# Performance work log

Measured on AMD Instinct MI355X. Metric: run time of the kernel, lower is better.

## Reference

```python
import jax, jax.numpy as jnp
import numpy as np

N_NODES = 50000
N_EDGES = 800000
IN_CH = 256
HID = 32
HEADS1 = 4
OUT_CH = 64
NEG_SLOPE = 0.2


def setup_inputs() -> dict:
    key = jax.random.key(0)
    ks = jax.random.split(key, 10)
    x = jax.random.normal(ks[0], (N_NODES, IN_CH), dtype=jnp.float32)
    edge_index = jax.random.randint(ks[1], (2, N_EDGES), 0, N_NODES, dtype=jnp.int64)
    g1 = float(np.sqrt(2.0 / (IN_CH + HEADS1 * HID)))
    g2 = float(np.sqrt(2.0 / (HEADS1 * HID + OUT_CH)))
    return {
        "x": x,
        "edge_index": edge_index,
        "W1": jax.random.normal(ks[2], (IN_CH, HEADS1 * HID), dtype=jnp.float32) * g1,
        "a_src1": jax.random.normal(ks[3], (HEADS1, HID), dtype=jnp.float32) * 0.1,
        "a_dst1": jax.random.normal(ks[4], (HEADS1, HID), dtype=jnp.float32) * 0.1,
        "b1": jnp.zeros((HEADS1 * HID,), dtype=jnp.float32),
        "W2": jax.random.normal(ks[5], (HEADS1 * HID, OUT_CH), dtype=jnp.float32) * g2,
        "a_src2": jax.random.normal(ks[6], (1, OUT_CH), dtype=jnp.float32) * 0.1,
        "a_dst2": jax.random.normal(ks[7], (1, OUT_CH), dtype=jnp.float32) * 0.1,
        "b2": jnp.zeros((OUT_CH,), dtype=jnp.float32),
    }


def gat_conv(x, src, dst, W, a_s, a_d, b, concat):
    # PyG-style GATConv: per-head linear, additive attention, edge softmax over dst,
    # scatter-add aggregation.
    N = x.shape[0]
    H, C = a_s.shape
    h = (x @ W).reshape(N, H, C)                    # [N, H, C]
    as_n = jnp.einsum("nhc,hc->nh", h, a_s)         # [N, H]
    ad_n = jnp.einsum("nhc,hc->nh", h, a_d)         # [N, H]
    e = jax.nn.leaky_relu(as_n[src] + ad_n[dst], NEG_SLOPE)  # [E, H]
    # segment softmax over incoming edges of each dst node
    m = jax.lax.stop_gradient(jax.ops.segment_max(e, dst, num_segments=N))
    ex = jnp.exp(e - m[dst])
    denom = jax.ops.segment_sum(ex, dst, num_segments=N)
    alpha = ex / (denom[dst] + 1e-16)               # [E, H]
    msg = h[src] * alpha[:, :, None]                # [E, H, C]
    out = jax.ops.segment_sum(msg, dst, num_segments=N)  # [N, H, C]
    out = out.reshape(N, H * C) if concat else out.mean(axis=1)
    return out + b


def reference(x, edge_index, W1, a_src1, a_dst1, b1, W2, a_src2, a_dst2, b2):
    # eval mode: dropout(p=0.5) is identity
    src, dst = edge_index[0], edge_index[1]
    h = gat_conv(x, src, dst, W1, a_src1, a_dst1, b1, concat=True)
    h = jax.nn.relu(h)
    return gat_conv(h, src, dst, W2, a_src2, a_dst2, b2, concat=False)
```

## Files before the change

### kernel.cpp

```cpp
#include <hip/hip_runtime.h>
#include <hip/hip_fp16.h>

#define N_NODES 50000
#define N_EDGES 800000
#define IN_CH   256
#define HID     32
#define HEADS1  4
#define C1      128
#define OUT_CH  64
#define NEG     0.2f
#define INVLN2  1.4426950408889634f
#define BSHIFT  10
#define NBKT    49
#define BCAP    17664
#define N1E     144
#define N2E     80

typedef _Float16 h8 __attribute__((ext_vector_type(8)));
typedef float f32x4 __attribute__((ext_vector_type(4)));

__global__ void k_prep(const float* __restrict__ W1, const float* __restrict__ W2,
                       const float* __restrict__ a_s1, const float* __restrict__ a_d1,
                       const float* __restrict__ a_s2, const float* __restrict__ a_d2,
                       _Float16* __restrict__ Wt1e, _Float16* __restrict__ Wt2e,
                       int* __restrict__ bcur) {
    int t = blockIdx.x * 256 + threadIdx.x;
    if (blockIdx.x == 0 && threadIdx.x < NBKT) bcur[threadIdx.x] = threadIdx.x * BCAP;
    if (t < 32768) {
        int c = t >> 8, k = t & 255;
        Wt1e[(size_t)c * 256 + k] = (_Float16)W1[(size_t)k * C1 + c];
    } else if (t < 34816) {
        int i = t - 32768;
        int k = i & 255, h = (i >> 8) & 3, which = i >> 10;
        const float* av = which ? a_d1 : a_s1;
        float s = 0.f;
        for (int c = 0; c < 32; ++c)
            s = fmaf(W1[(size_t)k * C1 + h * 32 + c], av[h * 32 + c], s);
        Wt1e[(size_t)(128 + which * 4 + h) * 256 + k] = (_Float16)(s * INVLN2);
    } else if (t < 36864) {
        int i = t - 34816;
        int k = i & 255, c = 136 + (i >> 8);
        Wt1e[(size_t)c * 256 + k] = (_Float16)0.f;
    } else if (t < 45056) {
        int i = t - 36864;
        int c = i >> 7, k = i & 127;
        Wt2e[(size_t)c * 128 + k] = (_Float16)W2[(size_t)k * OUT_CH + c];
    } else if (t < 45312) {
        int i = t - 45056;
        int k = i & 127, which = i >> 7;
        const float* av = which ? a_d2 : a_s2;
        float s = 0.f;
        for (int c = 0; c < 64; ++c)
            s = fmaf(W2[(size_t)k * OUT_CH + c], av[c], s);
        Wt2e[(size_t)(64 + which) * 128 + k] = (_Float16)(s * INVLN2);
    } else if (t < 47104) {
        int i = t - 45312;
        int k = i & 127, c = 66 + (i >> 7);
        Wt2e[(size_t)c * 128 + k] = (_Float16)0.f;
    }
}

__global__ __launch_bounds__(512) void gemm1_mfma(const float* __restrict__ X,
                                                  const _Float16* __restrict__ Wt1e,
                                                  __half* __restrict__ H,
                                                  float* __restrict__ as_n,
                                                  float* __restrict__ ad_n) {
    __shared__ _Float16 As[128 * 40];
    __shared__ _Float16 Bt[N1E * 40];
    const int tid = threadIdx.x;
    const int w = tid >> 6, lane = tid & 63;
    const int row0 = blockIdx.x * 128;
    const int lr = lane & 15, lk = (lane >> 4) * 8;
    const int ar = tid >> 2, aks = (tid & 3) * 8;
    const int gr_a = row0 + ar;
    const bool arow_ok = gr_a < N_NODES;
    const int bc = tid >> 1, bq = tid & 1;
    const bool bcol_ok = tid < 2 * N1E;

    f32x4 acc[9];
#pragma unroll
    for (int n = 0; n < 9; ++n) acc[n] = (f32x4){0.f, 0.f, 0.f, 0.f};

    float4 av0 = make_float4(0.f, 0.f, 0.f, 0.f), av1 = av0;
    h8 bv0 = {}, bv1 = {};
    if (arow_ok) {
        av0 = *(const float4*)(X + (size_t)gr_a * IN_CH + aks);
        av1 = *(const float4*)(X + (size_t)gr_a * IN_CH + aks + 4);
    }
    if (bcol_ok) {
        const h8* wp = (const h8*)(Wt1e + (size_t)bc * IN_CH + bq * 16);
        bv0 = wp[0];
        bv1 = wp[1];
    }

    for (int kk = 0; kk < IN_CH; kk += 32) {
        {
            h8 hv;
            hv[0] = (_Float16)av0.x; hv[1] = (_Float16)av0.y;
            hv[2] = (_Float16)av0.z; hv[3] = (_Float16)av0.w;
            hv[4] = (_Float16)av1.x; hv[5] = (_Float16)av1.y;
            hv[6] = (_Float16)av1.z; hv[7] = (_Float16)av1.w;
            *(h8*)(&As[ar * 40 + aks]) = hv;
            if (bcol_ok) {
                *(h8*)(&Bt[bc * 40 + bq * 16]) = bv0;
                *(h8*)(&Bt[bc * 40 + bq * 16 + 8]) = bv1;
            }
        }
        __syncthreads();
        int kn = kk + 32;
        if (kn < IN_CH) {
            if (arow_ok) {
                av0 = *(const float4*)(X + (size_t)gr_a * IN_CH + kn + aks);
                av1 = *(const float4*)(X + (size_t)gr_a * IN_CH + kn + aks + 4);
            }
            if (bcol_ok) {
                const h8* wp = (const h8*)(Wt1e + (size_t)bc * IN_CH + kn + bq * 16);
                bv0 = wp[0];
                bv1 = wp[1];
            }
        }
        h8 a = *(const h8*)(&As[(w * 16 + lr) * 40 + lk]);
#pragma unroll
        for (int n = 0; n < 9; ++n) {
            h8 b = *(const h8*)(&Bt[(n * 16 + lr) * 40 + lk]);
            acc[n] = __builtin_amdgcn_mfma_f32_16x16x32_f16(a, b, acc[n], 0, 0, 0);
        }
        __syncthreads();
    }
#pragma unroll
    for (int n = 0; n < 8; ++n)
#pragma unroll
        for (int j = 0; j < 4; ++j) {
            int gr = row0 + w * 16 + (lane >> 4) * 4 + j;
            if (gr < N_NODES) H[(size_t)gr * C1 + n * 16 + lr] = __float2half(acc[n][j]);
        }
#pragma unroll
    for (int j = 0; j < 4; ++j) {
        int gr = row0 + w * 16 + (lane >> 4) * 4 + j;
        if (gr < N_NODES) {
            if (lr < 4) as_n[gr * 4 + lr] = acc[8][j];
            else if (lr < 8) ad_n[gr * 4 + (lr - 4)] = acc[8][j];
        }
    }
}

__global__ __launch_bounds__(512) void gemm2_mfma(const __half* __restrict__ A,
                                                  const _Float16* __restrict__ Wt2e,
                                                  __half* __restrict__ H,
                                                  float* __restrict__ as_n,
                                                  float* __restrict__ ad_n) {
    __shared__ _Float16 Bt[N2E * 136];
    const int tid = threadIdx.x;
    const int w = tid >> 6, lane = tid & 63;
    const int row0 = blockIdx.x * 128;
    const int lr = lane & 15, lk = (lane >> 4) * 8;
    if (tid < 160) {
        int c = tid >> 1, q = tid & 1;
        const h8* wp = (const h8*)(Wt2e + (size_t)c * C1 + q * 64);
#pragma unroll
        for (int j = 0; j < 8; ++j)
            *(h8*)(&Bt[c * 136 + q * 64 + j * 8]) = wp[j];
    }
    __syncthreads();
    f32x4 acc[5];
#pragma unroll
    for (int n = 0; n < 5; ++n) acc[n] = (f32x4){0.f, 0.f, 0.f, 0.f};
    int grow = row0 + w * 16 + lr;
    grow = grow < N_NODES ? grow : N_NODES - 1;
    const _Float16* Ah = (const _Float16*)A;
#pragma unroll
    for (int kk = 0; kk < C1; kk += 32) {
        h8 a = *(const h8*)(Ah + (size_t)grow * C1 + kk + lk);
#pragma unroll
        for (int n = 0; n < 5; ++n) {
            h8 b = *(const h8*)(&Bt[(n * 16 + lr) * 136 + kk + lk]);
            acc[n] = __builtin_amdgcn_mfma_f32_16x16x32_f16(a, b, acc[n], 0, 0, 0);
        }
    }
#pragma unroll
    for (int n = 0; n < 4; ++n)
#pragma unroll
        for (int j = 0; j < 4; ++j) {
            int gr = row0 + w * 16 + (lane >> 4) * 4 + j;
            if (gr < N_NODES) H[(size_t)gr * OUT_CH + n * 16 + lr] = __float2half(acc[n][j]);
        }
#pragma unroll
    for (int j = 0; j < 4; ++j) {
        int gr = row0 + w * 16 + (lane >> 4) * 4 + j;
        if (gr < N_NODES) {
            if (lr == 0) as_n[gr] = acc[4][j];
            else if (lr == 1) ad_n[gr] = acc[4][j];
        }
    }
}

__global__ __launch_bounds__(256) void k_bucket(const int* __restrict__ src,
                                                const int* __restrict__ dst,
                                                int* __restrict__ bcur,
                                                int* __restrict__ pairs) {
    __shared__ int cnt[4 * NBKT];
    __shared__ int base[4 * NBKT];
    const int t = threadIdx.x;
    const int w = t >> 6;
    for (int i = t; i < 4 * NBKT; i += 256) cnt[i] = 0;
    __syncthreads();
    const int e0 = blockIdx.x * 2048 + t * 8;
    int s[8], d[8], r[8];
    bool valid = e0 + 7 < N_EDGES;
    if (valid) {
        int4 sa = *(const int4*)(src + e0);
        int4 sb = *(const int4*)(src + e0 + 4);
        int4 da = *(const int4*)(dst + e0);
        int4 db = *(const int4*)(dst + e0 + 4);
        s[0] = sa.x; s[1] = sa.y; s[2] = sa.z; s[3] = sa.w;
        s[4] = sb.x; s[5] = sb.y; s[6] = sb.z; s[7] = sb.w;
        d[0] = da.x; d[1] = da.y; d[2] = da.z; d[3] = da.w;
        d[4] = db.x; d[5] = db.y; d[6] = db.z; d[7] = db.w;
#pragma unroll
        for (int k = 0; k < 8; ++k)
            r[k] = atomicAdd(&cnt[w * NBKT + (d[k] >> BSHIFT)], 1);
    }
    __syncthreads();
    if (t < NBKT) {
        int c0 = cnt[0 * NBKT + t], c1 = cnt[1 * NBKT + t];
        int c2 = cnt[2 * NBKT + t], c3 = cnt[3 * NBKT + t];
        int g = atomicAdd(&bcur[t], c0 + c1 + c2 + c3);
        base[0 * NBKT + t] = g;
        base[1 * NBKT + t] = g + c0;
        base[2 * NBKT + t] = g + c0 + c1;
        base[3 * NBKT + t] = g + c0 + c1 + c2;
    }
    __syncthreads();
    if (valid) {
#pragma unroll
        for (int k = 0; k < 8; ++k) {
            int bin = d[k] >> BSHIFT;
            int pos = base[w * NBKT + bin] + r[k];
            if (pos < (bin + 1) * BCAP)
                pairs[pos] = ((d[k] & 1023) << 16) | s[k];
        }
    }
}

__global__ __launch_bounds__(256) void k_csr(const int* __restrict__ pairs,
                                             const int* __restrict__ bcur,
                                             int* __restrict__ estart,
                                             int* __restrict__ eend,
                                             int* __restrict__ esrc) {
    __shared__ int hist[1024];
    __shared__ int cur[1024];
    __shared__ int s[256];
    const int b = blockIdx.x;
    const int t = threadIdx.x;
#pragma unroll
    for (int k = t; k < 1024; k += 256) hist[k] = 0;
    __syncthreads();
    int cnt = bcur[b] - b * BCAP;
    if (cnt > BCAP) cnt = BCAP;
    const int* p = pairs + (size_t)b * BCAP;
    const int cnt4 = cnt & ~3;
    for (int i = t * 4; i < cnt4; i += 1024) {
        int4 v = *(const int4*)(p + i);
        atomicAdd(&hist[v.x >> 16], 1);
        atomicAdd(&hist[v.y >> 16], 1);
        atomicAdd(&hist[v.z >> 16], 1);
        atomicAdd(&hist[v.w >> 16], 1);
    }
    for (int i = cnt4 + t; i < cnt; i += 256)
        atomicAdd(&hist[p[i] >> 16], 1);
    __syncthreads();
    int h0 = hist[4 * t], h1 = hist[4 * t + 1], h2 = hist[4 * t + 2], h3 = hist[4 * t + 3];
    int sum = h0 + h1 + h2 + h3;
    s[t] = sum;
    __syncthreads();
#pragma unroll
    for (int o = 1; o < 256; o <<= 1) {
        int v = (t >= o) ? s[t - o] : 0;
        __syncthreads();
        s[t] += v;
        __syncthreads();
    }
    int excl = s[t] - sum;
    int gbase = b * BCAP + excl;
    cur[4 * t]     = gbase;
    cur[4 * t + 1] = gbase + h0;
    cur[4 * t + 2] = gbase + h0 + h1;
    cur[4 * t + 3] = gbase + h0 + h1 + h2;
    const int nbase = b << BSHIFT;
#pragma unroll
    for (int i = 0; i < 4; ++i) {
        int node = nbase + 4 * t + i;
        if (node < N_NODES) {
            int st = cur[4 * t + i];
            estart[node] = st;
            eend[node] = st + hist[4 * t + i];
        }
    }
    __syncthreads();
    for (int i = t * 4; i < cnt4; i += 1024) {
        int4 v = *(const int4*)(p + i);
        esrc[atomicAdd(&cur[v.x >> 16], 1)] = v.x & 0xFFFF;
        esrc[atomicAdd(&cur[v.y >> 16], 1)] = v.y & 0xFFFF;
        esrc[atomicAdd(&cur[v.z >> 16], 1)] = v.z & 0xFFFF;
        esrc[atomicAdd(&cur[v.w >> 16], 1)] = v.w & 0xFFFF;
    }
    for (int i = cnt4 + t; i < cnt; i += 256) {
        int v = p[i];
        esrc[atomicAdd(&cur[v >> 16], 1)] = v & 0xFFFF;
    }
}

__global__ __launch_bounds__(256) void gat_aggr1_csr(const int* __restrict__ estart,
                                                     const int* __restrict__ eend,
                                                     const int* __restrict__ esrc,
                                                     const float* __restrict__ as1,
                                                     const float* __restrict__ ad1,
                                                     const __half* __restrict__ h1,
                                                     const float* __restrict__ b1,
                                                     __half* __restrict__ hrelu) {
    int n = blockIdx.x * 4 + (threadIdx.x >> 6);
    if (n >= N_NODES) return;
    const int lane = threadIdx.x & 63;
    const int q = lane >> 4, li = lane & 15;
    const int head = li >> 2;
    const int c0 = li * 8;
    const int base = estart[n];
    const int end = eend[n];
    const float ad = ad1[n * 4 + head];
    const _Float16* __restrict__ H = (const _Float16*)h1;
    float den0 = 0.f, den1 = 0.f;
    float acc0[8], acc1[8];
#pragma unroll
    for (int k = 0; k < 8; ++k) { acc0[k] = 0.f; acc1[k] = 0.f; }

    for (int b0 = base; b0 < end; b0 += 64) {
        int cnt = end - b0; if (cnt > 64) cnt = 64;
        int myidx = (lane < cnt) ? esrc[b0 + lane] : 0;
        for (int it = 0; it < cnt; it += 8) {
            int j0 = it + q * 2, j1 = j0 + 1;
            bool p0 = j0 < cnt, p1 = j1 < cnt;
            int s0 = __shfl(myidx, p0 ? j0 : 0);
            int s1 = __shfl(myidx, p1 ? j1 : 0);
            float x0 = as1[s0 * 4 + head] + ad;
            x0 = x0 > 0.f ? x0 : NEG * x0;
            float w0 = p0 ? exp2f(x0) : 0.f;
            float x1 = as1[s1 * 4 + head] + ad;
            x1 = x1 > 0.f ? x1 : NEG * x1;
            float w1 = p1 ? exp2f(x1) : 0.f;
            h8 hv0 = *(const h8*)(H + (size_t)s0 * C1 + c0);
            h8 hv1 = *(const h8*)(H + (size_t)s1 * C1 + c0);
            den0 += w0;
            den1 += w1;
#pragma unroll
            for (int k = 0; k < 8; ++k) {
                acc0[k] = fmaf((float)hv0[k], w0, acc0[k]);
                acc1[k] = fmaf((float)hv1[k], w1, acc1[k]);
            }
        }
    }
    float den = den0 + den1;
    float r[8];
#pragma unroll
    for (int k = 0; k < 8; ++k) r[k] = acc0[k] + acc1[k];
    den += __shfl_xor(den, 16);
    den += __shfl_xor(den, 32);
#pragma unroll
    for (int k = 0; k < 8; ++k) {
        r[k] += __shfl_xor(r[k], 16);
        r[k] += __shfl_xor(r[k], 32);
    }
    if (q == 0) {
        float4 bb0 = *(const float4*)(b1 + c0);
        float4 bb1 = *(const float4*)(b1 + c0 + 4);
        float bv[8] = {bb0.x, bb0.y, bb0.z, bb0.w, bb1.x, bb1.y, bb1.z, bb1.w};
        float inv = 1.f / (den + 1e-16f);
        h8 o;
#pragma unroll
        for (int k = 0; k < 8; ++k) {
            float v = fmaf(r[k], inv, bv[k]);
            o[k] = (_Float16)(v > 0.f ? v : 0.f);
        }
        *(h8*)((_Float16*)hrelu + (size_t)n * C1 + c0) = o;
    }
}

__global__ __launch_bounds__(256) void gat_aggr2_csr(const int* __restrict__ estart,
                                                     const int* __restrict__ eend,
                                                     const int* __restrict__ esrc,
                                                     const float* __restrict__ as2,
                                                     const float* __restrict__ ad2,
                                                     const __half* __restrict__ h2,
                                                     const float* __restrict__ b2,
                                                     float* __restrict__ out) {
    int n = blockIdx.x * 4 + (threadIdx.x >> 6);
    if (n >= N_NODES) return;
    const int lane = threadIdx.x & 63;
    const int q = lane >> 3, li = lane & 7;
    const int c0 = li * 8;
    const int base = estart[n];
    const int end = eend[n];
    const float ad = ad2[n];
    const _Float16* __restrict__ H = (const _Float16*)h2;
    float den0 = 0.f, den1 = 0.f;
    float acc0[8], acc1[8];
#pragma unroll
    for (int k = 0; k < 8; ++k) { acc0[k] = 0.f; acc1[k] = 0.f; }

    for (int b0 = base; b0 < end; b0 += 64) {
        int cnt = end - b0; if (cnt > 64) cnt = 64;
        int myidx = (lane < cnt) ? esrc[b0 + lane] : 0;
        for (int it = 0; it < cnt; it += 16) {
            int j0 = it + q * 2, j1 = j0 + 1;
            bool p0 = j0 < cnt, p1 = j1 < cnt;
            int s0 = __shfl(myidx, p0 ? j0 : 0);
            int s1 = __shfl(myidx, p1 ? j1 : 0);
            float x0 = as2[s0] + ad;
            x0 = x0 > 0.f ? x0 : NEG * x0;
            float w0 = p0 ? exp2f(x0) : 0.f;
            float x1 = as2[s1] + ad;
            x1 = x1 > 0.f ? x1 : NEG * x1;
            float w1 = p1 ? exp2f(x1) : 0.f;
            h8 hv0 = *(const h8*)(H + (size_t)s0 * OUT_CH + c0);
            h8 hv1 = *(const h8*)(H + (size_t)s1 * OUT_CH + c0);
            den0 += w0;
            den1 += w1;
#pragma unroll
            for (int k = 0; k < 8; ++k) {
                acc0[k] = fmaf((float)hv0[k], w0, acc0[k]);
                acc1[k] = fmaf((float)hv1[k], w1, acc1[k]);
            }
        }
    }
    float den = den0 + den1;
    float r[8];
#pragma unroll
    for (int k = 0; k < 8; ++k) r[k] = acc0[k] + acc1[k];
    den += __shfl_xor(den, 8);
    den += __shfl_xor(den, 16);
    den += __shfl_xor(den, 32);
#pragma unroll
    for (int k = 0; k < 8; ++k) {
        r[k] += __shfl_xor(r[k], 8);
        r[k] += __shfl_xor(r[k], 16);
        r[k] += __shfl_xor(r[k], 32);
    }
    if (q == 0) {
        float4 bb0 = *(const float4*)(b2 + c0);
        float4 bb1 = *(const float4*)(b2 + c0 + 4);
        float inv = 1.f / (den + 1e-16f);
        float4 o0, o1;
        o0.x = fmaf(r[0], inv, bb0.x);
        o0.y = fmaf(r[1], inv, bb0.y);
        o0.z = fmaf(r[2], inv, bb0.z);
        o0.w = fmaf(r[3], inv, bb0.w);
        o1.x = fmaf(r[4], inv, bb1.x);
        o1.y = fmaf(r[5], inv, bb1.y);
        o1.z = fmaf(r[6], inv, bb1.z);
        o1.w = fmaf(r[7], inv, bb1.w);
        *(float4*)(out + (size_t)n * OUT_CH + c0) = o0;
        *(float4*)(out + (size_t)n * OUT_CH + c0 + 4) = o1;
    }
}

extern "C" void kernel_launch(void* const* d_in, const int* in_sizes, int n_in,
                              void* d_out, int out_size, void* d_ws, size_t ws_size,
                              hipStream_t stream) {
    const float* x      = (const float*)d_in[0];
    const int*   ei     = (const int*)d_in[1];
    const float* W1     = (const float*)d_in[2];
    const float* a_src1 = (const float*)d_in[3];
    const float* a_dst1 = (const float*)d_in[4];
    const float* b1     = (const float*)d_in[5];
    const float* W2     = (const float*)d_in[6];
    const float* a_src2 = (const float*)d_in[7];
    const float* a_dst2 = (const float*)d_in[8];
    const float* b2     = (const float*)d_in[9];
    float* out = (float*)d_out;

    const int* src = ei;
    const int* dst = ei + N_EDGES;

    char* w = (char*)d_ws;
    auto carve = [&](size_t bytes) {
        char* p = w;
        w += (bytes + 255) & ~(size_t)255;
        return p;
    };
    __half*   h1     = (__half*)carve((size_t)N_NODES * C1 * 2);
    __half*   hrelu  = (__half*)carve((size_t)N_NODES * C1 * 2);
    float*    as1    = (float*)carve((size_t)N_NODES * 4 * 4);
    float*    ad1    = (float*)carve((size_t)N_NODES * 4 * 4);
    int*      estart = (int*)carve((size_t)N_NODES * 4);
    int*      eend   = (int*)carve((size_t)N_NODES * 4);
    int*      esrc   = (int*)carve((size_t)NBKT * BCAP * 4);
    int*      bcur   = (int*)carve((size_t)NBKT * 4);
    int*      pairs  = (int*)carve((size_t)NBKT * BCAP * 4);
    _Float16* Wt1e   = (_Float16*)carve((size_t)N1E * IN_CH * 2);
    _Float16* Wt2e   = (_Float16*)carve((size_t)N2E * C1 * 2);

    __half* h2  = h1;
    float*  as2 = as1;
    float*  ad2 = ad1;

    k_prep<<<184, 256, 0, stream>>>(W1, W2, a_src1, a_dst1, a_src2, a_dst2,
                                    Wt1e, Wt2e, bcur);
    k_bucket<<<(N_EDGES + 2047) / 2048, 256, 0, stream>>>(src, dst, bcur, pairs);
    k_csr<<<NBKT, 256, 0, stream>>>(pairs, bcur, estart, eend, esrc);

    gemm1_mfma<<<(N_NODES + 127) / 128, 512, 0, stream>>>(x, Wt1e, h1, as1, ad1);
    gat_aggr1_csr<<<(N_NODES + 3) / 4, 256, 0, stream>>>(estart, eend, esrc, as1, ad1, h1, b1, hrelu);

    gemm2_mfma<<<(N_NODES + 127) / 128, 512, 0, stream>>>(hrelu, Wt2e, h2, as2, ad2);
    gat_aggr2_csr<<<(N_NODES + 3) / 4, 256, 0, stream>>>(estart, eend, esrc, as2, ad2, h2, b2, out);

    (void)in_sizes; (void)n_in; (void)out_size; (void)ws_size;
}
```

Baseline: 130.3 us.

## Sort nodes by in-degree within buckets to balance aggregation wavefronts

The CSR build now also computes, per 1024-node bucket, a permutation of nodes ordered by in-degree (capped at 63) using a shared-memory counting sort. Both aggregation kernels read their node id from this permutation, so the four wavefronts in a block and neighbouring blocks handle nodes of similar degree, which reduces divergence in the per-node edge loops and tail imbalance. In exchange, k_csr does extra syncs and writes a permutation array, the aggregation kernels take one more indirection, and output writes become scattered. Padding slots launch wavefronts that exit immediately.

New measurement: 134.7 us. 1.03x slower.

```diff
diff --git a/kernel.cpp b/kernel.cpp
--- a/kernel.cpp
+++ b/kernel.cpp
@@ -15,6 +15,7 @@
 #define BCAP    17664
 #define N1E     144
 #define N2E     80
+#define NPERM   (NBKT * 1024)
 
 typedef _Float16 h8 __attribute__((ext_vector_type(8)));
 typedef float f32x4 __attribute__((ext_vector_type(4)));
@@ -246,10 +247,13 @@
                                              const int* __restrict__ bcur,
                                              int* __restrict__ estart,
                                              int* __restrict__ eend,
-                                             int* __restrict__ esrc) {
+                                             int* __restrict__ esrc,
+                                             int* __restrict__ perm) {
     __shared__ int hist[1024];
     __shared__ int cur[1024];
     __shared__ int s[256];
+    __shared__ int dh[64];
+    __shared__ int dcur[64];
     const int b = blockIdx.x;
     const int t = threadIdx.x;
 #pragma unroll
@@ -296,6 +300,41 @@
             eend[node] = st + hist[4 * t + i];
         }
     }
+    if (t < 64) dh[t] = 0;
+    int mydeg[4];
+#pragma unroll
+    for (int i = 0; i < 4; ++i) {
+        int node = nbase + 4 * t + i;
+        int dgi = hist[4 * t + i];
+        mydeg[i] = (node < N_NODES) ? (dgi < 63 ? dgi : 63) : -1;
+    }
+    __syncthreads();
+#pragma unroll
+    for (int i = 0; i < 4; ++i)
+        if (mydeg[i] >= 0) atomicAdd(&dh[mydeg[i]], 1);
+    perm[b * 1024 + t] = -1;
+    perm[b * 1024 + 256 + t] = -1;
+    perm[b * 1024 + 512 + t] = -1;
+    perm[b * 1024 + 768 + t] = -1;
+    __syncthreads();
+    if (t < 64) s[t] = dh[t];
+    __syncthreads();
+#pragma unroll
+    for (int o = 1; o < 64; o <<= 1) {
+        int v = (t >= o && t < 64) ? s[t - o] : 0;
+        __syncthreads();
+        if (t < 64) s[t] += v;
+        __syncthreads();
+    }
+    if (t < 64) dcur[t] = s[t] - dh[t];
+    __syncthreads();
+#pragma unroll
+    for (int i = 0; i < 4; ++i) {
+        if (mydeg[i] >= 0) {
+            int pos = atomicAdd(&dcur[mydeg[i]], 1);
+            perm[b * 1024 + pos] = nbase + 4 * t + i;
+        }
+    }
     __syncthreads();
     for (int i = t * 4; i < cnt4; i += 1024) {
         int4 v = *(const int4*)(p + i);
@@ -310,7 +349,8 @@
     }
 }
 
-__global__ __launch_bounds__(256) void gat_aggr1_csr(const int* __restrict__ estart,
+__global__ __launch_bounds__(256) void gat_aggr1_csr(const int* __restrict__ perm,
+                                                     const int* __restrict__ estart,
                                                      const int* __restrict__ eend,
                                                      const int* __restrict__ esrc,
                                                      const float* __restrict__ as1,
@@ -318,8 +358,8 @@
                                                      const __half* __restrict__ h1,
                                                      const float* __restrict__ b1,
                                                      __half* __restrict__ hrelu) {
-    int n = blockIdx.x * 4 + (threadIdx.x >> 6);
-    if (n >= N_NODES) return;
+    int n = perm[blockIdx.x * 4 + (threadIdx.x >> 6)];
+    if (n < 0) return;
     const int lane = threadIdx.x & 63;
     const int q = lane >> 4, li = lane & 15;
     const int head = li >> 2;
@@ -384,7 +424,8 @@
     }
 }
 
-__global__ __launch_bounds__(256) void gat_aggr2_csr(const int* __restrict__ estart,
+__global__ __launch_bounds__(256) void gat_aggr2_csr(const int* __restrict__ perm,
+                                                     const int* __restrict__ estart,
                                                      const int* __restrict__ eend,
                                                      const int* __restrict__ esrc,
                                                      const float* __restrict__ as2,
@@ -392,8 +433,8 @@
                                                      const __half* __restrict__ h2,
                                                      const float* __restrict__ b2,
                                                      float* __restrict__ out) {
-    int n = blockIdx.x * 4 + (threadIdx.x >> 6);
-    if (n >= N_NODES) return;
+    int n = perm[blockIdx.x * 4 + (threadIdx.x >> 6)];
+    if (n < 0) return;
     const int lane = threadIdx.x & 63;
     const int q = lane >> 3, li = lane & 7;
     const int c0 = li * 8;
@@ -495,6 +536,7 @@
     int*      esrc   = (int*)carve((size_t)NBKT * BCAP * 4);
     int*      bcur   = (int*)carve((size_t)NBKT * 4);
     int*      pairs  = (int*)carve((size_t)NBKT * BCAP * 4);
+    int*      perm   = (int*)carve((size_t)NPERM * 4);
     _Float16* Wt1e   = (_Float16*)carve((size_t)N1E * IN_CH * 2);
     _Float16* Wt2e   = (_Float16*)carve((size_t)N2E * C1 * 2);
 
@@ -505,13 +547,13 @@
     k_prep<<<184, 256, 0, stream>>>(W1, W2, a_src1, a_dst1, a_src2, a_dst2,
                                     Wt1e, Wt2e, bcur);
     k_bucket<<<(N_EDGES + 2047) / 2048, 256, 0, stream>>>(src, dst, bcur, pairs);
-    k_csr<<<NBKT, 256, 0, stream>>>(pairs, bcur, estart, eend, esrc);
+    k_csr<<<NBKT, 256, 0, stream>>>(pairs, bcur, estart, eend, esrc, perm);
 
     gemm1_mfma<<<(N_NODES + 127) / 128, 512, 0, stream>>>(x, Wt1e, h1, as1, ad1);
-    gat_aggr1_csr<<<(N_NODES + 3) / 4, 256, 0, stream>>>(estart, eend, esrc, as1, ad1, h1, b1, hrelu);
+    gat_aggr1_csr<<<NPERM / 4, 256, 0, stream>>>(perm, estart, eend, esrc, as1, ad1, h1, b1, hrelu);
 
     gemm2_mfma<<<(N_NODES + 127) / 128, 512, 0, stream>>>(hrelu, Wt2e, h2, as2, ad2);
-    gat_aggr2_csr<<<(N_NODES + 3) / 4, 256, 0, stream>>>(estart, eend, esrc, as2, ad2, h2, b2, out);
+    gat_aggr2_csr<<<NPERM / 4, 256, 0, stream>>>(perm, estart, eend, esrc, as2, ad2, h2, b2, out);
 
     (void)in_sizes; (void)n_in; (void)out_size; (void)ws_size;
 }
```
